# Optimization experiments

Hardware: AMD Instinct MI355X
Metric: run time of the kernel (lower is better)

The kernel has to match this reference:

```python
import jax, jax.numpy as jnp
import numpy as np


def _average(x, w, W):
    """layers.Average forward: weighted mean over batch of Linear(x) (bias=False).
    x: [N, d_in], w: [N, 1], W: [d_out, d_in] -> [1, d_out]"""
    h = x @ W.T                                    # [N, d_out]
    return jnp.sum(h * w, axis=0, keepdims=True) / jnp.sum(w)


def setup_inputs() -> dict:
    key = jax.random.key(0)
    k1, k2, k3, k4 = jax.random.split(key, 4)
    N, n_in, n_middle = 1_000_000, 32, 128
    x = jax.random.normal(k1, (N, n_in), dtype=jnp.float32)
    w = jax.random.uniform(k2, (N, 1), dtype=jnp.float32)
    # Linear weights (Kaiming-ish scale), bias=False per __init__ default
    W_in = jax.random.normal(k3, (n_middle, n_in), dtype=jnp.float32) / np.float32(np.sqrt(n_in))
    W_out = jax.random.normal(k4, (n_in, n_middle), dtype=jnp.float32) / np.float32(np.sqrt(n_middle))
    return {"x": x, "w": w, "W_in": W_in, "W_out": W_out}


def reference(x, w, W_in, W_out):
    # x_ = activation(avg_in(x, w))
    h = jax.nn.relu(_average(x, w, W_in))          # [1, n_middle]
    # x_ = avg_out(x_, w); residual add (broadcast over batch)
    x_ = _average(h, w, W_out)                     # [1, n_in]
    return x + x_                                  # [N, n_in]
```

## Files before the change

### kernel.cpp

```cpp
#include <hip/hip_runtime.h>

#define BS 256
#define NB1 2048
#define NB3 2048

typedef float vfloat4 __attribute__((ext_vector_type(4)));

__global__ void __launch_bounds__(BS) reduce_kernel(
    const float* __restrict__ x, const float* __restrict__ w,
    float* __restrict__ colpart, float* __restrict__ wpart, long long total4) {
  const int tid = threadIdx.x;
  const long long stride2 = (long long)gridDim.x * (2 * BS);
  const vfloat4* x4 = (const vfloat4*)x;
  vfloat4 a0 = (vfloat4)(0.f);
  vfloat4 a1 = (vfloat4)(0.f);
  float w0 = 0.f, w1 = 0.f;
  long long c = (long long)blockIdx.x * (2 * BS) + tid;
  for (; c + BS < total4; c += stride2) {
    const float wi0 = w[(int)(c >> 3)];
    const float wi1 = w[(int)((c + BS) >> 3)];
    const vfloat4 v0 = x4[c];
    const vfloat4 v1 = x4[c + BS];
    a0 += wi0 * v0;
    a1 += wi1 * v1;
    w0 += wi0; w1 += wi1;
  }
  if (c < total4) {
    const float wi = w[(int)(c >> 3)];
    a0 += wi * x4[c];
    w0 += wi;
  }
  a0 += a1;
  w0 += w1;
  __shared__ vfloat4 sacc[BS];
  __shared__ float   sw[BS];
  sacc[tid] = a0;
  sw[tid] = w0;
  __syncthreads();
  for (int s = BS / 2; s >= 8; s >>= 1) {
    if (tid < s) {
      sacc[tid] += sacc[tid + s];
      sw[tid] += sw[tid + s];
    }
    __syncthreads();
  }
  if (tid < 8) {
    ((vfloat4*)(colpart + (long long)blockIdx.x * 32))[tid] = sacc[tid];
  }
  if (tid == 0) {
    wpart[blockIdx.x] = sw[0] + sw[1] + sw[2] + sw[3] +
                        sw[4] + sw[5] + sw[6] + sw[7];
  }
}

__global__ void __launch_bounds__(BS) middle_kernel(
    const float* __restrict__ colpart, const float* __restrict__ wpart,
    const float* __restrict__ W_in, const float* __restrict__ W_out,
    float* __restrict__ r_out, int nb) {
  const int tid = threadIdx.x;
  __shared__ vfloat4 sacc[BS];
  __shared__ float   swr[BS];
  __shared__ float   avg[32];
  __shared__ float   h[128];
  {
    const vfloat4* cp4 = (const vfloat4*)colpart;
    const int nchunk = nb * 8;
    vfloat4 acc = (vfloat4)(0.f);
    for (int cb = tid; cb < nchunk; cb += BS) acc += cp4[cb];
    sacc[tid] = acc;
  }
  {
    const vfloat4* wp4 = (const vfloat4*)wpart;
    const int nchunk = nb / 4;
    float s = 0.f;
    for (int cb = tid; cb < nchunk; cb += BS) {
      vfloat4 v = wp4[cb];
      s += v.x + v.y + v.z + v.w;
    }
    swr[tid] = s;
  }
  __syncthreads();
  for (int s = BS / 2; s >= 8; s >>= 1) {
    if (tid < s) {
      sacc[tid] += sacc[tid + s];
      swr[tid] += swr[tid + s];
    }
    __syncthreads();
  }
  if (tid == 0) {
    float wsum = (swr[0] + swr[1] + swr[2] + swr[3] +
                  swr[4] + swr[5] + swr[6] + swr[7]) * 0.125f;
    swr[0] = wsum;
  }
  __syncthreads();
  if (tid < 32) {
    const float* sflat = (const float*)sacc;
    avg[tid] = sflat[tid] / swr[0];
  }
  __syncthreads();
  if (tid < 128) {
    float a = 0.f;
    for (int k = 0; k < 32; ++k) a = fmaf(W_in[tid * 32 + k], avg[k], a);
    h[tid] = fmaxf(a, 0.f);
  }
  __syncthreads();
  if (tid < 32) {
    float r = 0.f;
    for (int k = 0; k < 128; ++k) r = fmaf(W_out[tid * 128 + k], h[k], r);
    r_out[tid] = r;
  }
}

__global__ void __launch_bounds__(BS) add_kernel(
    const float* __restrict__ x, const float* __restrict__ r,
    float* __restrict__ out, long long total4) {
  const int tid = threadIdx.x;
  const vfloat4 rr = ((const vfloat4*)r)[tid & 7];
  const long long stride2 = (long long)gridDim.x * (2 * BS);
  const vfloat4* x4 = (const vfloat4*)x;
  vfloat4* o4 = (vfloat4*)out;
  long long c = (long long)blockIdx.x * (2 * BS) + tid;
  for (; c + BS < total4; c += stride2) {
    vfloat4 v0 = x4[c] + rr;
    vfloat4 v1 = x4[c + BS] + rr;
    __builtin_nontemporal_store(v0, &o4[c]);
    __builtin_nontemporal_store(v1, &o4[c + BS]);
  }
  if (c < total4) {
    vfloat4 v = x4[c] + rr;
    __builtin_nontemporal_store(v, &o4[c]);
  }
}

extern "C" void kernel_launch(void* const* d_in, const int* in_sizes, int n_in,
                              void* d_out, int out_size, void* d_ws, size_t ws_size,
                              hipStream_t stream) {
  const float* x     = (const float*)d_in[0];
  const float* w     = (const float*)d_in[1];
  const float* W_in  = (const float*)d_in[2];
  const float* W_out = (const float*)d_in[3];
  float* out = (float*)d_out;

  const long long N = (long long)in_sizes[0] / 32;
  const long long total4 = N * 8;

  int nb = NB1;
  while (nb > 64 && (size_t)(nb * 33 + 32) * 4 > ws_size) nb >>= 1;
  float* colpart = (float*)d_ws;
  float* wpart   = colpart + (size_t)nb * 32;
  float* r       = wpart + nb;

  reduce_kernel<<<nb, BS, 0, stream>>>(x, w, colpart, wpart, total4);
  middle_kernel<<<1, BS, 0, stream>>>(colpart, wpart, W_in, W_out, r, nb);
  add_kernel<<<NB3, BS, 0, stream>>>(x, r, out, total4);
}
```

Baseline: 265.7 us.

## Fuse reduce, middle and add into one cooperative kernel with grid sync

Replaces the three-kernel pipeline with a single cooperative kernel. Each of 1024 blocks reduces two virtual blocks of partials, then a grid-wide sync follows, after which every block redundantly computes the small MLP into shared memory and runs the residual add. This removes two kernel launches and the global round-trip for r. The cost is a grid sync and each block re-reading all partials. The old path is kept as a fallback if the cooperative launch fails.

```diff
diff --git a/kernel.cpp b/kernel.cpp
--- a/kernel.cpp
+++ b/kernel.cpp
@@ -1,10 +1,132 @@
 #include <hip/hip_runtime.h>
-
-#define BS 256
-#define NB1 2048
-#define NB3 2048
+#include <hip/hip_cooperative_groups.h>
+
+namespace cg = cooperative_groups;
+
+#define BS   256
+#define GRID 1024
+#define VNB  2048
+#define NB3  2048
 
 typedef float vfloat4 __attribute__((ext_vector_type(4)));
+
+__global__ void __launch_bounds__(BS) fused_kernel(
+    const float* __restrict__ x, const float* __restrict__ w,
+    const float* __restrict__ W_in, const float* __restrict__ W_out,
+    float* __restrict__ out, float* __restrict__ colpart,
+    float* __restrict__ wpart, long long total4) {
+  const int tid = threadIdx.x;
+  __shared__ vfloat4 sacc[BS];
+  __shared__ float   swr[BS];
+  __shared__ float   avg[32];
+  __shared__ float   h[128];
+  __shared__ __align__(16) float sr[32];
+
+  {
+    const vfloat4* x4 = (const vfloat4*)x;
+    const long long stride2 = (long long)VNB * (2 * BS);
+    for (int half = 0; half < 2; ++half) {
+      const int vb = (int)blockIdx.x + half * GRID;
+      vfloat4 a0 = (vfloat4)(0.f), a1 = (vfloat4)(0.f);
+      float w0 = 0.f, w1 = 0.f;
+      long long c = (long long)vb * (2 * BS) + tid;
+      for (; c + BS < total4; c += stride2) {
+        const float wi0 = w[(int)(c >> 3)];
+        const float wi1 = w[(int)((c + BS) >> 3)];
+        const vfloat4 v0 = x4[c];
+        const vfloat4 v1 = x4[c + BS];
+        a0 += wi0 * v0;
+        a1 += wi1 * v1;
+        w0 += wi0; w1 += wi1;
+      }
+      if (c < total4) {
+        const float wi = w[(int)(c >> 3)];
+        a0 += wi * x4[c];
+        w0 += wi;
+      }
+      a0 += a1;
+      w0 += w1;
+      __syncthreads();
+      sacc[tid] = a0;
+      swr[tid]  = w0;
+      __syncthreads();
+      for (int s = BS / 2; s >= 8; s >>= 1) {
+        if (tid < s) { sacc[tid] += sacc[tid + s]; swr[tid] += swr[tid + s]; }
+        __syncthreads();
+      }
+      if (tid < 8) {
+        ((vfloat4*)(colpart + (long long)vb * 32))[tid] = sacc[tid];
+      }
+      if (tid == 0) {
+        wpart[vb] = swr[0] + swr[1] + swr[2] + swr[3] +
+                    swr[4] + swr[5] + swr[6] + swr[7];
+      }
+    }
+  }
+
+  cg::this_grid().sync();
+
+  {
+    const vfloat4* cp4 = (const vfloat4*)colpart;
+    vfloat4 acc = (vfloat4)(0.f);
+    for (int cb = tid; cb < VNB * 8; cb += BS) acc += cp4[cb];
+    sacc[tid] = acc;
+    {
+      const vfloat4* wp4 = (const vfloat4*)wpart;
+      float s = 0.f;
+      for (int cb = tid; cb < VNB / 4; cb += BS) {
+        vfloat4 v = wp4[cb];
+        s += v.x + v.y + v.z + v.w;
+      }
+      swr[tid] = s;
+    }
+    __syncthreads();
+    for (int s = BS / 2; s >= 8; s >>= 1) {
+      if (tid < s) { sacc[tid] += sacc[tid + s]; swr[tid] += swr[tid + s]; }
+      __syncthreads();
+    }
+    if (tid == 0) {
+      swr[0] = (swr[0] + swr[1] + swr[2] + swr[3] +
+                swr[4] + swr[5] + swr[6] + swr[7]) * 0.125f;
+    }
+    __syncthreads();
+    if (tid < 32) {
+      const float* sflat = (const float*)sacc;
+      avg[tid] = sflat[tid] / swr[0];
+    }
+    __syncthreads();
+    if (tid < 128) {
+      float a = 0.f;
+      for (int k = 0; k < 32; ++k) a = fmaf(W_in[tid * 32 + k], avg[k], a);
+      h[tid] = fmaxf(a, 0.f);
+    }
+    __syncthreads();
+    if (tid < 32) {
+      float rv = 0.f;
+      for (int k = 0; k < 128; ++k) rv = fmaf(W_out[tid * 128 + k], h[k], rv);
+      sr[tid] = rv;
+    }
+    __syncthreads();
+  }
+
+  {
+    const vfloat4 rr = ((const vfloat4*)sr)[tid & 7];
+    const long long stride2 = (long long)GRID * (2 * BS);
+    const vfloat4* x4 = (const vfloat4*)x;
+    vfloat4* o4 = (vfloat4*)out;
+    long long c = (long long)blockIdx.x * (2 * BS) + tid;
+    for (; c + BS < total4; c += stride2) {
+      vfloat4 v0 = x4[c] + rr;
+      vfloat4 v1 = x4[c + BS] + rr;
+      __builtin_nontemporal_store(v0, &o4[c]);
+      __builtin_nontemporal_store(v1, &o4[c + BS]);
+    }
+    if (c < total4) {
+      vfloat4 v = x4[c] + rr;
+      __builtin_nontemporal_store(v, &o4[c]);
+    }
+  }
+}
 
 __global__ void __launch_bounds__(BS) reduce_kernel(
     const float* __restrict__ x, const float* __restrict__ w,
@@ -38,19 +160,12 @@
   sw[tid] = w0;
   __syncthreads();
   for (int s = BS / 2; s >= 8; s >>= 1) {
-    if (tid < s) {
-      sacc[tid] += sacc[tid + s];
-      sw[tid] += sw[tid + s];
-    }
-    __syncthreads();
-  }
-  if (tid < 8) {
-    ((vfloat4*)(colpart + (long long)blockIdx.x * 32))[tid] = sacc[tid];
-  }
-  if (tid == 0) {
-    wpart[blockIdx.x] = sw[0] + sw[1] + sw[2] + sw[3] +
-                        sw[4] + sw[5] + sw[6] + sw[7];
-  }
+    if (tid < s) { sacc[tid] += sacc[tid + s]; sw[tid] += sw[tid + s]; }
+    __syncthreads();
+  }
+  if (tid < 8) ((vfloat4*)(colpart + (long long)blockIdx.x * 32))[tid] = sacc[tid];
+  if (tid == 0)
+    wpart[blockIdx.x] = sw[0] + sw[1] + sw[2] + sw[3] + sw[4] + sw[5] + sw[6] + sw[7];
 }
 
 __global__ void __launch_bounds__(BS) middle_kernel(
@@ -81,16 +196,12 @@
   }
   __syncthreads();
   for (int s = BS / 2; s >= 8; s >>= 1) {
-    if (tid < s) {
-      sacc[tid] += sacc[tid + s];
-      swr[tid] += swr[tid + s];
-    }
+    if (tid < s) { sacc[tid] += sacc[tid + s]; swr[tid] += swr[tid + s]; }
     __syncthreads();
   }
   if (tid == 0) {
-    float wsum = (swr[0] + swr[1] + swr[2] + swr[3] +
-                  swr[4] + swr[5] + swr[6] + swr[7]) * 0.125f;
-    swr[0] = wsum;
+    swr[0] = (swr[0] + swr[1] + swr[2] + swr[3] +
+              swr[4] + swr[5] + swr[6] + swr[7]) * 0.125f;
   }
   __syncthreads();
   if (tid < 32) {
@@ -144,12 +255,20 @@
   const long long N = (long long)in_sizes[0] / 32;
   const long long total4 = N * 8;
 
-  int nb = NB1;
+  float* colpart = (float*)d_ws;
+  float* wpart   = colpart + (size_t)VNB * 32;
+  float* r       = wpart + VNB;
+
+  if ((size_t)(VNB * 33 + 32) * 4 <= ws_size) {
+    void* args[] = {(void*)&x, (void*)&w, (void*)&W_in, (void*)&W_out,
+                    (void*)&out, (void*)&colpart, (void*)&wpart, (void*)&total4};
+    hipError_t err = hipLaunchCooperativeKernel((const void*)fused_kernel,
+                                                dim3(GRID), dim3(BS), args, 0, stream);
+    if (err == hipSuccess) return;
+  }
+
+  int nb = VNB;
   while (nb > 64 && (size_t)(nb * 33 + 32) * 4 > ws_size) nb >>= 1;
-  float* colpart = (float*)d_ws;
-  float* wpart   = colpart + (size_t)nb * 32;
-  float* r       = wpart + nb;
-
   reduce_kernel<<<nb, BS, 0, stream>>>(x, w, colpart, wpart, total4);
   middle_kernel<<<1, BS, 0, stream>>>(colpart, wpart, W_in, W_out, r, nb);
   add_kernel<<<NB3, BS, 0, stream>>>(x, r, out, total4);
```

After: 345.3 us. 29.9% more time.
